# Performance work log

Hardware: AMD Instinct MI355X
Metric: run time of the kernel (lower is better)

The kernel has to match this reference:

```python
import jax, jax.numpy as jnp
import numpy as np

LN_EPS = 1e-12


def _layernorm(x, gamma, beta):
    mu = jnp.mean(x, axis=-1, keepdims=True)
    var = jnp.var(x, axis=-1, keepdims=True)
    return gamma * (x - mu) / jnp.sqrt(var + LN_EPS) + beta


def setup_inputs() -> dict:
    key = jax.random.key(0)
    ks = jax.random.split(key, 8)
    B, N, C, H = 8, 8192, 512, 8
    FFN = 4 * C
    s_attn = 1.0 / np.sqrt(C)
    s_ffn1 = 1.0 / np.sqrt(C)
    s_ffn2 = 1.0 / np.sqrt(FFN)
    return {
        "x": jax.random.normal(ks[0], (B, N, C), jnp.float32),
        "wq": jax.random.normal(ks[1], (C, C), jnp.float32) * s_attn,
        "bq": jnp.zeros((C,), jnp.float32),
        "wk": jax.random.normal(ks[2], (C, C), jnp.float32) * s_attn,
        "bk": jnp.zeros((C,), jnp.float32),
        "wv": jax.random.normal(ks[3], (C, C), jnp.float32) * s_attn,
        "bv": jnp.zeros((C,), jnp.float32),
        "wo": jax.random.normal(ks[4], (C, C), jnp.float32) * s_attn,
        "bo": jnp.zeros((C,), jnp.float32),
        "gamma1": jnp.ones((C,), jnp.float32),
        "beta1": jnp.zeros((C,), jnp.float32),
        "w_fc1": jax.random.normal(ks[5], (C, FFN), jnp.float32) * s_ffn1,
        "b_fc1": jnp.zeros((FFN,), jnp.float32),
        "w_fc2": jax.random.normal(ks[6], (FFN, C), jnp.float32) * s_ffn2,
        "b_fc2": jnp.zeros((C,), jnp.float32),
        "gamma2": jnp.ones((C,), jnp.float32),
        "beta2": jnp.zeros((C,), jnp.float32),
        "window_size": 64,
        "n_head": 8,
    }


def reference(x, wq, bq, wk, bk, wv, bv, wo, bo, gamma1, beta1,
              w_fc1, b_fc1, w_fc2, b_fc2, gamma2, beta2,
              window_size, n_head):
    B, N, C = x.shape
    ws = window_size
    H = n_head
    dh = C // H

    # window partition: [B, N, C] -> [B*N/ws, ws, C]
    xw = x.reshape(B * N // ws, ws, C)
    shortcut = xw

    # windowed multi-head self-attention
    q = (xw @ wq + bq).reshape(-1, ws, H, dh)
    k = (xw @ wk + bk).reshape(-1, ws, H, dh)
    v = (xw @ wv + bv).reshape(-1, ws, H, dh)
    scale = 1.0 / jnp.sqrt(jnp.asarray(dh, xw.dtype))
    attn = jnp.einsum('wqhd,wkhd->whqk', q, k) * scale  # [nw, H, ws, ws]
    attn = jax.nn.softmax(attn, axis=-1)
    out = jnp.einsum('whqk,wkhd->wqhd', attn, v).reshape(-1, ws, C)
    out = out @ wo + bo

    # residual + LN1
    h = _layernorm(out + shortcut, gamma1, beta1)

    # MLP (fc1 -> GELU -> fc2), residual + LN2
    ff = jax.nn.gelu(h @ w_fc1 + b_fc1, approximate=False) @ w_fc2 + b_fc2
    h = _layernorm(ff + h, gamma2, beta2)

    # window reverse: -> [B, N, C]
    return h.reshape(B, N, C)
```

## Files before the change

### kernel.cpp

```cpp
#include <hip/hip_runtime.h>

typedef __attribute__((ext_vector_type(8))) short bf16x8;
typedef __attribute__((ext_vector_type(4))) float f32x4;

__device__ __forceinline__ short f2b(float f) {
  unsigned u = __builtin_bit_cast(unsigned, f);
  unsigned r = (u + 0x7FFFu + ((u >> 16) & 1u)) >> 16;
  return (short)r;
}
__device__ __forceinline__ float b2f(short s) {
  unsigned u = ((unsigned)(unsigned short)s) << 16;
  return __builtin_bit_cast(float, u);
}

__device__ __forceinline__ void gload16(const void* g, void* l) {
  __builtin_amdgcn_global_load_lds(
      (const __attribute__((address_space(1))) void*)g,
      (__attribute__((address_space(3))) void*)l, 16, 0, 0);
}

__device__ __forceinline__ float gelu_f(float v) {
  float u = v * (0.7978845608f + 0.0356774081f * v * v);
  float a = fabsf(u);
  float e = __expf(-2.f * a);
  float t = (1.f - e) * __builtin_amdgcn_rcpf(1.f + e);
  t = (u < 0.f) ? -t : t;
  return 0.5f * v * (1.f + t);
}

__global__ void cvt_bf16_vec(const float* __restrict__ src, short* __restrict__ dst, long n) {
  long i = ((long)blockIdx.x * 256 + threadIdx.x) * 8;
  if (i >= n) return;
  f32x4 a = *(const f32x4*)(src + i);
  f32x4 b = *(const f32x4*)(src + i + 4);
  bf16x8 o;
#pragma unroll
  for (int j = 0; j < 4; j++) o[j] = f2b(a[j]);
#pragma unroll
  for (int j = 0; j < 4; j++) o[j + 4] = f2b(b[j]);
  *(bf16x8*)(dst + i) = o;
}

__global__ void transpose_cvt_t(const float* __restrict__ src, short* __restrict__ dst,
                                int K, int N) {
  __shared__ float tile[32][33];
  const int n0 = blockIdx.x * 32, k0 = blockIdx.y * 32;
  const int j = threadIdx.x & 31, i0 = threadIdx.x >> 5;
#pragma unroll
  for (int r = 0; r < 4; r++) {
    int i = i0 + r * 8;
    tile[i][j] = src[(long)(k0 + i) * N + n0 + j];
  }
  __syncthreads();
#pragma unroll
  for (int r = 0; r < 4; r++) {
    int i = i0 + r * 8;
    dst[(long)(n0 + i) * K + k0 + j] = f2b(tile[j][i]);
  }
}

__global__ void pack_bias3(const float* __restrict__ b0, const float* __restrict__ b1,
                           const float* __restrict__ b2, float* __restrict__ out) {
  int t = blockIdx.x * 256 + threadIdx.x;
  if (t >= 1536) return;
  out[t] = (t < 512) ? b0[t] : ((t < 1024) ? b1[t - 512] : b2[t - 1024]);
}

#define DSR(d, a, OFF) \
  asm volatile("ds_read_b128 %0, %1 offset:" OFF : "=v"(d) : "v"(a))
#define SB __builtin_amdgcn_sched_barrier(0)

template <int EPI>
__global__ __launch_bounds__(512, 1) void gemm256(
    const short* __restrict__ A, const short* __restrict__ Bt,
    const float* __restrict__ bias, const float* __restrict__ resF,
    const short* __restrict__ resB, void* __restrict__ Cout, int K, int ldc, int gxN) {
  extern __shared__ short lds[];
  const int t = threadIdx.x;
  const int lane = t & 63, w = t >> 6;
  const int lr = lane & 15, lg = lane >> 4;
  const int wm = w >> 2, wn = w & 3;

  const int nwg = gridDim.x, orig = blockIdx.x;
  const int q8 = nwg >> 3, r8 = nwg & 7, xcd = orig & 7, idx = orig >> 3;
  const int swz = (xcd < r8 ? xcd * (q8 + 1) : r8 * (q8 + 1) + (xcd - r8) * q8) + idx;
  const long m0 = (long)(swz / gxN) * 256;
  const int n0 = (swz % gxN) * 256;

  f32x4 acc[8][4];
#pragma unroll
  for (int i = 0; i < 8; i++)
#pragma unroll
    for (int j = 0; j < 4; j++) acc[i][j] = f32x4{0.f, 0.f, 0.f, 0.f};

  const int srow = t >> 3;
  const int sch = (t & 7) ^ (srow & 7);
  const short* sA = A + (m0 + srow) * (long)K + sch * 8;
  const short* sB = Bt + ((long)n0 + srow) * K + sch * 8;
  const long r64 = (long)64 * K;

#define STG_A(tt, h)                                                     \
  {                                                                      \
    short* d_ = lds + ((tt) & 1) * 16384 + (h) * 8192 + t * 8;           \
    const short* s_ = sA + (h) * 2 * r64 + (long)(tt) * 64;              \
    gload16(s_, d_);                                                     \
    gload16(s_ + r64, d_ + 4096);                                        \
  }
#define STG_B(tt, h)                                                     \
  {                                                                      \
    short* d_ = lds + 32768 + ((tt) & 1) * 16384 + (h) * 8192 + t * 8;   \
    const short* s_ = sB + (h) * 2 * r64 + (long)(tt) * 64;              \
    gload16(s_, d_);                                                     \
    gload16(s_ + r64, d_ + 4096);                                        \
  }

  const unsigned ldsB = (unsigned)(uintptr_t)lds;
  const unsigned xb0 = (unsigned)((lg ^ (lr & 7)) * 16);
  const unsigned xb1 = (unsigned)(((4 + lg) ^ (lr & 7)) * 16);
  const unsigned aRowB = (unsigned)((wm * 128 + lr) * 128);
  const unsigned bRowB = 65536u + (unsigned)((wn * 64 + lr) * 128);

#define BAR                                  \
  {                                          \
    SB;                                      \
    __builtin_amdgcn_s_barrier();            \
    SB;                                      \
  }
#define LGKM0 asm volatile("s_waitcnt lgkmcnt(0)")

  const int NT = K >> 6;
  STG_A(0, 0) STG_A(0, 1) STG_B(0, 0) STG_B(0, 1) STG_B(1, 0) STG_B(1, 1)
  asm volatile("s_waitcnt vmcnt(4)" ::: "memory");
  BAR

#define MFMA8(AC, A0, A1)                                                      \
  {                                                                            \
    __builtin_amdgcn_s_setprio(1);                                             \
    acc[AC][0] = __builtin_amdgcn_mfma_f32_16x16x32_bf16(A0, b00, acc[AC][0], 0, 0, 0); \
    acc[AC][0] = __builtin_amdgcn_mfma_f32_16x16x32_bf16(A1, b01, acc[AC][0], 0, 0, 0); \
    acc[AC][1] = __builtin_amdgcn_mfma_f32_16x16x32_bf16(A0, b10, acc[AC][1], 0, 0, 0); \
    acc[AC][1] = __builtin_amdgcn_mfma_f32_16x16x32_bf16(A1, b11, acc[AC][1], 0, 0, 0); \
    acc[AC][2] = __builtin_amdgcn_mfma_f32_16x16x32_bf16(A0, b20, acc[AC][2], 0, 0, 0); \
    acc[AC][2] = __builtin_amdgcn_mfma_f32_16x16x32_bf16(A1, b21, acc[AC][2], 0, 0, 0); \
    acc[AC][3] = __builtin_amdgcn_mfma_f32_16x16x32_bf16(A0, b30, acc[AC][3], 0, 0, 0); \
    acc[AC][3] = __builtin_amdgcn_mfma_f32_16x16x32_bf16(A1, b31, acc[AC][3], 0, 0, 0); \
    __builtin_amdgcn_s_setprio(0);                                             \
  }

  for (int tt = 0; tt < NT; ++tt) {
    const unsigned dAb = (unsigned)((tt & 1) * 32768);
    const unsigned aA0 = ldsB + aRowB + xb0 + dAb;
    const unsigned aA1 = ldsB + aRowB + xb1 + dAb;
    const unsigned bA0 = ldsB + bRowB + xb0 + dAb;
    const unsigned bA1 = ldsB + bRowB + xb1 + dAb;
    bf16x8 b00, b01, b10, b11, b20, b21, b30, b31;

    {
      DSR(b00, bA0, "0");    DSR(b01, bA1, "0");
      DSR(b10, bA0, "2048"); DSR(b11, bA1, "2048");
      DSR(b20, bA0, "4096"); DSR(b21, bA1, "4096");
      DSR(b30, bA0, "6144"); DSR(b31, bA1, "6144");
      bf16x8 a00, a01, a10, a11;
      DSR(a00, aA0, "0");    DSR(a01, aA1, "0");
      DSR(a10, aA0, "2048"); DSR(a11, aA1, "2048");
      SB;
      if (tt + 1 < NT) STG_A(tt + 1, 0)
      BAR
      LGKM0; SB;
      MFMA8(0, a00, a01)
      MFMA8(1, a10, a11)
      BAR
    }
    {
      bf16x8 a00, a01, a10, a11;
      DSR(a00, aA0, "4096"); DSR(a01, aA1, "4096");
      DSR(a10, aA0, "6144"); DSR(a11, aA1, "6144");
      SB;
      if (tt + 1 < NT) STG_A(tt + 1, 1)
      BAR
      LGKM0; SB;
      MFMA8(2, a00, a01)
      MFMA8(3, a10, a11)
      BAR
    }
    {
      bf16x8 a00, a01, a10, a11;
      DSR(a00, aA0, "8192");  DSR(a01, aA1, "8192");
      DSR(a10, aA0, "10240"); DSR(a11, aA1, "10240");
      SB;
      if (tt + 2 < NT) STG_B(tt + 2, 0)
      BAR
      LGKM0; SB;
      MFMA8(4, a00, a01)
      MFMA8(5, a10, a11)
      BAR
    }
    {
      bf16x8 a00, a01, a10, a11;
      DSR(a00, aA0, "12288"); DSR(a01, aA1, "12288");
      DSR(a10, aA0, "14336"); DSR(a11, aA1, "14336");
      SB;
      if (tt + 2 < NT) STG_B(tt + 2, 1)
      BAR
      LGKM0; SB;
      MFMA8(6, a00, a01)
      MFMA8(7, a10, a11)
      if (tt + 2 < NT) {
        asm volatile("s_waitcnt vmcnt(4)" ::: "memory");
      } else if (tt + 1 < NT) {
        asm volatile("s_waitcnt vmcnt(0)" ::: "memory");
      }
      BAR
    }
  }
#undef MFMA8
#undef STG_A
#undef STG_B

  float bv[4];
#pragma unroll
  for (int nj = 0; nj < 4; nj++) bv[nj] = bias[n0 + wn * 64 + nj * 16 + lr];

#pragma unroll
  for (int a = 0; a < 8; a++)
#pragma unroll
    for (int i = 0; i < 4; i++) {
      const long row = m0 + wm * 128 + a * 16 + lg * 4 + i;
      const long rb = row * ldc + n0 + wn * 64 + lr;
      if (EPI == 0) {
        short* p = (short*)Cout + rb;
#pragma unroll
        for (int nj = 0; nj < 4; nj++) p[nj * 16] = f2b(acc[a][nj][i] + bv[nj]);
      } else if (EPI == 1) {
        short* p = (short*)Cout + rb;
#pragma unroll
        for (int nj = 0; nj < 4; nj++) p[nj * 16] = f2b(gelu_f(acc[a][nj][i] + bv[nj]));
      } else if (EPI == 2) {
        float* p = (float*)Cout + rb;
        const float* rp = resF + rb;
#pragma unroll
        for (int nj = 0; nj < 4; nj++) p[nj * 16] = acc[a][nj][i] + bv[nj] + rp[nj * 16];
      } else {
        float* p = (float*)Cout + rb;
        const short* rp = resB + rb;
#pragma unroll
        for (int nj = 0; nj < 4; nj++)
          p[nj * 16] = acc[a][nj][i] + bv[nj] + b2f(rp[nj * 16]);
      }
    }
}
#undef DSR
#undef SB
#undef BAR
#undef LGKM0

__global__ __launch_bounds__(256, 2) void attn_win(const short* __restrict__ QKV,
                                                   short* __restrict__ AO) {
  __shared__ short Vs[64 * 72];
  __shared__ short Ps[64 * 72];
  const int t = threadIdx.x, w = t >> 6, lane = t & 63;
  const int lr = lane & 15, lg = lane >> 4;
  const long base = (long)blockIdx.x * 64 * 1536;
  const long obase = (long)blockIdx.x * 64 * 512;

  for (int h = 0; h < 8; h++) {
    const int co = h * 64;
#pragma unroll
    for (int it = 0; it < 2; it++) {
      int c = t + it * 256;
      int j = c >> 3, d0 = (c & 7) * 8;
      *(bf16x8*)(Vs + j * 72 + d0) =
          *(const bf16x8*)(QKV + base + (long)j * 1536 + 1024 + co + d0);
    }
    __syncthreads();

    bf16x8 qf[2], kf[4][2];
#pragma unroll
    for (int kb = 0; kb < 2; kb++)
      qf[kb] = *(const bf16x8*)(QKV + base + (long)(w * 16 + lr) * 1536 + co + kb * 32 + lg * 8);
#pragma unroll
    for (int nj = 0; nj < 4; nj++)
#pragma unroll
      for (int kb = 0; kb < 2; kb++)
        kf[nj][kb] = *(const bf16x8*)(QKV + base + (long)(nj * 16 + lr) * 1536 + 512 + co +
                                      kb * 32 + lg * 8);

    f32x4 s[4];
#pragma unroll
    for (int nj = 0; nj < 4; nj++) {
      s[nj] = f32x4{0.f, 0.f, 0.f, 0.f};
      s[nj] = __builtin_amdgcn_mfma_f32_16x16x32_bf16(qf[0], kf[nj][0], s[nj], 0, 0, 0);
      s[nj] = __builtin_amdgcn_mfma_f32_16x16x32_bf16(qf[1], kf[nj][1], s[nj], 0, 0, 0);
      s[nj] = s[nj] * 0.125f;
    }

#pragma unroll
    for (int i = 0; i < 4; i++) {
      float mx = fmaxf(fmaxf(s[0][i], s[1][i]), fmaxf(s[2][i], s[3][i]));
#pragma unroll
      for (int off = 1; off < 16; off <<= 1) mx = fmaxf(mx, __shfl_xor(mx, off, 64));
      float sum = 0.f;
#pragma unroll
      for (int nj = 0; nj < 4; nj++) {
        float p = __expf(s[nj][i] - mx);
        s[nj][i] = p;
        sum += p;
      }
#pragma unroll
      for (int off = 1; off < 16; off <<= 1) sum += __shfl_xor(sum, off, 64);
      float inv = 1.f / sum;
#pragma unroll
      for (int nj = 0; nj < 4; nj++) s[nj][i] *= inv;
    }

#pragma unroll
    for (int nj = 0; nj < 4; nj++)
#pragma unroll
      for (int i = 0; i < 4; i++)
        Ps[(w * 16 + lg * 4 + i) * 72 + nj * 16 + lr] = f2b(s[nj][i]);

    bf16x8 pa[2];
#pragma unroll
    for (int kb = 0; kb < 2; kb++)
      pa[kb] = *(const bf16x8*)(Ps + (w * 16 + lr) * 72 + kb * 32 + lg * 8);

    f32x4 o[4];
#pragma unroll
    for (int nb = 0; nb < 4; nb++) o[nb] = f32x4{0.f, 0.f, 0.f, 0.f};
#pragma unroll
    for (int kb = 0; kb < 2; kb++)
#pragma unroll
      for (int nb = 0; nb < 4; nb++) {
        bf16x8 vb;
#pragma unroll
        for (int jj = 0; jj < 8; jj++)
          vb[jj] = Vs[(kb * 32 + lg * 8 + jj) * 72 + nb * 16 + lr];
        o[nb] = __builtin_amdgcn_mfma_f32_16x16x32_bf16(pa[kb], vb, o[nb], 0, 0, 0);
      }

#pragma unroll
    for (int nb = 0; nb < 4; nb++)
#pragma unroll
      for (int i = 0; i < 4; i++)
        AO[obase + (long)(w * 16 + lg * 4 + i) * 512 + co + nb * 16 + lr] = f2b(o[nb][i]);
    __syncthreads();
  }
}

template <int OUTB>
__global__ __launch_bounds__(256, 4) void ln_rows(const float* __restrict__ Y,
                                                  const float* __restrict__ gamma,
                                                  const float* __restrict__ beta,
                                                  short* __restrict__ Hb,
                                                  float* __restrict__ Of) {
  const int w = threadIdx.x >> 6, lane = threadIdx.x & 63;
  const long row = (long)blockIdx.x * 4 + w;
  const float* y = Y + row * 512 + lane * 8;
  f32x4 a = *(const f32x4*)(y);
  f32x4 b = *(const f32x4*)(y + 4);
  float s = a[0] + a[1] + a[2] + a[3] + b[0] + b[1] + b[2] + b[3];
  float s2 = a[0] * a[0] + a[1] * a[1] + a[2] * a[2] + a[3] * a[3] + b[0] * b[0] +
             b[1] * b[1] + b[2] * b[2] + b[3] * b[3];
#pragma unroll
  for (int off = 1; off < 64; off <<= 1) {
    s += __shfl_xor(s, off, 64);
    s2 += __shfl_xor(s2, off, 64);
  }
  float mu = s * (1.f / 512.f);
  float var = s2 * (1.f / 512.f) - mu * mu;
  float rstd = rsqrtf(fmaxf(var, 0.f) + 1e-12f);
  const int c0 = lane * 8;
  f32x4 ga = *(const f32x4*)(gamma + c0), gb = *(const f32x4*)(gamma + c0 + 4);
  f32x4 ba = *(const f32x4*)(beta + c0), bb = *(const f32x4*)(beta + c0 + 4);
  if (OUTB) {
    bf16x8 o;
#pragma unroll
    for (int j = 0; j < 4; j++) o[j] = f2b(ga[j] * ((a[j] - mu) * rstd) + ba[j]);
#pragma unroll
    for (int j = 0; j < 4; j++) o[j + 4] = f2b(gb[j] * ((b[j] - mu) * rstd) + bb[j]);
    *(bf16x8*)(Hb + row * 512 + c0) = o;
  } else {
    f32x4 o0, o1;
#pragma unroll
    for (int j = 0; j < 4; j++) o0[j] = ga[j] * ((a[j] - mu) * rstd) + ba[j];
#pragma unroll
    for (int j = 0; j < 4; j++) o1[j] = gb[j] * ((b[j] - mu) * rstd) + bb[j];
    *(f32x4*)(Of + row * 512 + c0) = o0;
    *(f32x4*)(Of + row * 512 + c0 + 4) = o1;
  }
}

extern "C" void kernel_launch(void* const* d_in, const int* in_sizes, int n_in,
                              void* d_out, int out_size, void* d_ws, size_t ws_size,
                              hipStream_t stream) {
  (void)in_sizes; (void)n_in; (void)out_size;
  const float* x = (const float*)d_in[0];
  const float* wq = (const float*)d_in[1];
  const float* bq = (const float*)d_in[2];
  const float* wk = (const float*)d_in[3];
  const float* bk = (const float*)d_in[4];
  const float* wv = (const float*)d_in[5];
  const float* bv = (const float*)d_in[6];
  const float* wo = (const float*)d_in[7];
  const float* bo = (const float*)d_in[8];
  const float* g1 = (const float*)d_in[9];
  const float* be1 = (const float*)d_in[10];
  const float* wfc1 = (const float*)d_in[11];
  const float* bfc1 = (const float*)d_in[12];
  const float* wfc2 = (const float*)d_in[13];
  const float* bfc2 = (const float*)d_in[14];
  const float* g2 = (const float*)d_in[15];
  const float* be2 = (const float*)d_in[16];

  const long T = 65536;
  char* ws = (char*)d_ws;

  short* WQKVT = (short*)(ws);
  short* WOT = WQKVT + 1536 * 512;
  short* WFC1T = WOT + 512 * 512;
  short* WFC2T = WFC1T + 2048 * 512;
  float* BQKV = (float*)(WFC2T + 512 * 2048);
  size_t woff = ((size_t)((char*)(BQKV + 1536) - ws) + 255) & ~(size_t)255;

  size_t avail = (ws_size > woff) ? (ws_size - woff) : 0;
  long Tc = T;
  while (Tc > 256 && (size_t)Tc * 7168 > avail) Tc >>= 1;
  const long nch = T / Tc;

  char* R0 = ws + woff;
  char* R1 = R0 + (size_t)Tc * 4096;
  char* R2 = R1 + (size_t)Tc * 2048;

  short* QKV = (short*)R0;
  float* Y1 = (float*)R0;
  short* FF1 = (short*)R0;
  short* XB = (short*)R1;
  short* AO = (short*)R1;
  float* Y2 = (float*)R1;
  short* H = (short*)R2;

  transpose_cvt_t<<<dim3(16, 16), 256, 0, stream>>>(wq, WQKVT, 512, 512);
  transpose_cvt_t<<<dim3(16, 16), 256, 0, stream>>>(wk, WQKVT + 512 * 512, 512, 512);
  transpose_cvt_t<<<dim3(16, 16), 256, 0, stream>>>(wv, WQKVT + 1024 * 512, 512, 512);
  transpose_cvt_t<<<dim3(16, 16), 256, 0, stream>>>(wo, WOT, 512, 512);
  transpose_cvt_t<<<dim3(64, 16), 256, 0, stream>>>(wfc1, WFC1T, 512, 2048);
  transpose_cvt_t<<<dim3(16, 64), 256, 0, stream>>>(wfc2, WFC2T, 2048, 512);
  pack_bias3<<<6, 256, 0, stream>>>(bq, bk, bv, BQKV);

  const size_t LDSB = 131072;
  for (long c = 0; c < nch; c++) {
    const long t0 = c * Tc;
    const int mb = (int)(Tc / 256);
    cvt_bf16_vec<<<(int)(Tc / 4), 256, 0, stream>>>(x + t0 * 512, XB, Tc * 512);
    gemm256<0><<<mb * 6, 512, LDSB, stream>>>(XB, WQKVT, BQKV, nullptr, nullptr,
                                              (void*)QKV, 512, 1536, 6);
    attn_win<<<(int)(Tc / 64), 256, 0, stream>>>(QKV, AO);
    gemm256<2><<<mb * 2, 512, LDSB, stream>>>(AO, WOT, bo, x + t0 * 512, nullptr,
                                              (void*)Y1, 512, 512, 2);
    ln_rows<1><<<(int)(Tc / 4), 256, 0, stream>>>(Y1, g1, be1, H, nullptr);
    gemm256<1><<<mb * 8, 512, LDSB, stream>>>(H, WFC1T, bfc1, nullptr, nullptr,
                                              (void*)FF1, 512, 2048, 8);
    gemm256<3><<<mb * 2, 512, LDSB, stream>>>(FF1, WFC2T, bfc2, nullptr, H, (void*)Y2,
                                              2048, 512, 2);
    ln_rows<0><<<(int)(Tc / 4), 256, 0, stream>>>(Y2, g2, be2, nullptr,
                                                  (float*)d_out + t0 * 512);
  }
}
```

Measured before the change: 772.0 us.

## Add 128x128 triple-buffered GEMM for FC1 and store pre-LN1 sum in bf16

Adds a new 256-thread GEMM with 128x128 tiles and a three-stage LDS ring fed by direct global-to-LDS loads, and uses it for the FC1 projection in place of the 256x256 kernel. The smaller tiles give more workgroups, aiming at better occupancy and load balance. The attention-output GEMM now writes the residual sum as bf16 instead of fp32, and LN1 reads bf16, which halves that intermediate's traffic. The cost is lower precision for the LN1 input.

```diff
diff --git a/kernel.cpp b/kernel.cpp
--- a/kernel.cpp
+++ b/kernel.cpp
@@ -64,6 +64,123 @@
   int t = blockIdx.x * 256 + threadIdx.x;
   if (t >= 1536) return;
   out[t] = (t < 512) ? b0[t] : ((t < 1024) ? b1[t - 512] : b2[t - 1024]);
+}
+
+template <int EPI>
+__global__ __launch_bounds__(256, 3) void gemm_bt(
+    const short* __restrict__ A, const short* __restrict__ Bt,
+    const float* __restrict__ bias, const float* __restrict__ resF,
+    const short* __restrict__ resB, void* __restrict__ Cout, int K, int ldc, int gxN) {
+  __shared__ short lds[3 * 8192];
+  const int t = threadIdx.x;
+  const int w = t >> 6, lane = t & 63;
+  const int lr = lane & 15, lg = lane >> 4;
+
+  const int nwg = gridDim.x;
+  const int orig = blockIdx.x;
+  const int q = nwg >> 3, r = nwg & 7, xcd = orig & 7, idx = orig >> 3;
+  const int swz = (xcd < r ? xcd * (q + 1) : r * (q + 1) + (xcd - r) * q) + idx;
+  const long m0 = (long)(swz / gxN) * 128;
+  const int n0 = (swz % gxN) * 128;
+
+  const int wm = (w >> 1) * 64, wn = (w & 1) * 64;
+
+  f32x4 acc[4][4];
+#pragma unroll
+  for (int i = 0; i < 4; i++)
+#pragma unroll
+    for (int j = 0; j < 4; j++) acc[i][j] = f32x4{0.f, 0.f, 0.f, 0.f};
+
+  const int srow = t >> 2;
+  const int schunk = (t & 3) ^ ((t >> 3) & 3);
+  const short* Ag = A + (m0 + srow) * (long)K + schunk * 8;
+  const short* Bg = Bt + ((long)n0 + srow) * K + schunk * 8;
+  const long half = (long)64 * K;
+
+#define STAGE(b, kt)                                   \
+  {                                                    \
+    short* d = lds + (b) * 8192 + t * 8;               \
+    gload16(Ag + (long)(kt) * 32, d);                  \
+    gload16(Ag + half + (long)(kt) * 32, d + 2048);    \
+    gload16(Bg + (long)(kt) * 32, d + 4096);           \
+    gload16(Bg + half + (long)(kt) * 32, d + 6144);    \
+  }
+
+  const int xsw = (lg ^ ((lr >> 1) & 3)) * 8;
+  const int aoff = (wm + lr) * 32 + xsw;
+  const int boff = 4096 + (wn + lr) * 32 + xsw;
+
+#define TILE_WAIT(WN)                                        \
+  asm volatile("s_waitcnt vmcnt(" #WN ")" ::: "memory");     \
+  __builtin_amdgcn_sched_barrier(0);                         \
+  __builtin_amdgcn_s_barrier();                              \
+  __builtin_amdgcn_sched_barrier(0);
+
+#define BODY(CB)                                                               \
+  {                                                                            \
+    const short* Lb = lds + (CB) * 8192;                                       \
+    bf16x8 a[4], b[4];                                                         \
+    _Pragma("unroll") for (int mi = 0; mi < 4; mi++)                           \
+        a[mi] = *(const bf16x8*)(Lb + aoff + mi * 512);                        \
+    _Pragma("unroll") for (int nj = 0; nj < 4; nj++)                           \
+        b[nj] = *(const bf16x8*)(Lb + boff + nj * 512);                        \
+    __builtin_amdgcn_s_setprio(1);                                             \
+    _Pragma("unroll") for (int mi = 0; mi < 4; mi++)                           \
+        _Pragma("unroll") for (int nj = 0; nj < 4; nj++) acc[mi][nj] =         \
+            __builtin_amdgcn_mfma_f32_16x16x32_bf16(a[mi], b[nj], acc[mi][nj], \
+                                                    0, 0, 0);                  \
+    __builtin_amdgcn_s_setprio(0);                                             \
+  }
+
+  const int NKT = K >> 5;
+  STAGE(0, 0)
+  STAGE(1, 1)
+
+  int cb = 0, sb = 2;
+  for (int kt = 0; kt < NKT - 1; ++kt) {
+    TILE_WAIT(4)
+    if (kt + 2 < NKT) STAGE(sb, kt + 2)
+    BODY(cb)
+    cb = (cb == 2) ? 0 : cb + 1;
+    sb = (sb == 2) ? 0 : sb + 1;
+  }
+  TILE_WAIT(0)
+  BODY(cb)
+#undef STAGE
+#undef TILE_WAIT
+#undef BODY
+
+  float bv[4];
+#pragma unroll
+  for (int nj = 0; nj < 4; nj++) bv[nj] = bias[n0 + wn + nj * 16 + lr];
+
+#pragma unroll
+  for (int mi = 0; mi < 4; mi++)
+#pragma unroll
+    for (int i = 0; i < 4; i++) {
+      const long row = m0 + wm + mi * 16 + lg * 4 + i;
+      const long rb = row * ldc + n0 + wn + lr;
+      if (EPI == 0) {
+        short* p = (short*)Cout + rb;
+#pragma unroll
+        for (int nj = 0; nj < 4; nj++) p[nj * 16] = f2b(acc[mi][nj][i] + bv[nj]);
+      } else if (EPI == 1) {
+        short* p = (short*)Cout + rb;
+#pragma unroll
+        for (int nj = 0; nj < 4; nj++) p[nj * 16] = f2b(gelu_f(acc[mi][nj][i] + bv[nj]));
+      } else if (EPI == 2) {
+        short* p = (short*)Cout + rb;
+        const float* rp = resF + rb;
+#pragma unroll
+        for (int nj = 0; nj < 4; nj++) p[nj * 16] = f2b(acc[mi][nj][i] + bv[nj] + rp[nj * 16]);
+      } else {
+        float* p = (float*)Cout + rb;
+        const short* rp = resB + rb;
+#pragma unroll
+        for (int nj = 0; nj < 4; nj++)
+          p[nj * 16] = acc[mi][nj][i] + bv[nj] + b2f(rp[nj * 16]);
+      }
+    }
 }
 
 #define DSR(d, a, OFF) \
@@ -236,10 +353,11 @@
 #pragma unroll
         for (int nj = 0; nj < 4; nj++) p[nj * 16] = f2b(gelu_f(acc[a][nj][i] + bv[nj]));
       } else if (EPI == 2) {
-        float* p = (float*)Cout + rb;
+        short* p = (short*)Cout + rb;
         const float* rp = resF + rb;
 #pragma unroll
-        for (int nj = 0; nj < 4; nj++) p[nj * 16] = acc[a][nj][i] + bv[nj] + rp[nj * 16];
+        for (int nj = 0; nj < 4; nj++)
+          p[nj * 16] = f2b(acc[a][nj][i] + bv[nj] + rp[nj * 16]);
       } else {
         float* p = (float*)Cout + rb;
         const short* rp = resB + rb;
@@ -347,20 +465,29 @@
   }
 }
 
-template <int OUTB>
-__global__ __launch_bounds__(256, 4) void ln_rows(const float* __restrict__ Y,
+template <int INB, int OUTB>
+__global__ __launch_bounds__(256, 4) void ln_rows(const float* __restrict__ Yf,
+                                                  const short* __restrict__ Yb,
                                                   const float* __restrict__ gamma,
                                                   const float* __restrict__ beta,
                                                   short* __restrict__ Hb,
                                                   float* __restrict__ Of) {
   const int w = threadIdx.x >> 6, lane = threadIdx.x & 63;
   const long row = (long)blockIdx.x * 4 + w;
-  const float* y = Y + row * 512 + lane * 8;
-  f32x4 a = *(const f32x4*)(y);
-  f32x4 b = *(const f32x4*)(y + 4);
-  float s = a[0] + a[1] + a[2] + a[3] + b[0] + b[1] + b[2] + b[3];
-  float s2 = a[0] * a[0] + a[1] * a[1] + a[2] * a[2] + a[3] * a[3] + b[0] * b[0] +
-             b[1] * b[1] + b[2] * b[2] + b[3] * b[3];
+  float v[8];
+  if (INB) {
+    bf16x8 x = *(const bf16x8*)(Yb + row * 512 + lane * 8);
+#pragma unroll
+    for (int j = 0; j < 8; j++) v[j] = b2f(x[j]);
+  } else {
+    f32x4 a = *(const f32x4*)(Yf + row * 512 + lane * 8);
+    f32x4 b = *(const f32x4*)(Yf + row * 512 + lane * 8 + 4);
+#pragma unroll
+    for (int j = 0; j < 4; j++) { v[j] = a[j]; v[j + 4] = b[j]; }
+  }
+  float s = 0.f, s2 = 0.f;
+#pragma unroll
+  for (int j = 0; j < 8; j++) { s += v[j]; s2 += v[j] * v[j]; }
 #pragma unroll
   for (int off = 1; off < 64; off <<= 1) {
     s += __shfl_xor(s, off, 64);
@@ -375,16 +502,16 @@
   if (OUTB) {
     bf16x8 o;
 #pragma unroll
-    for (int j = 0; j < 4; j++) o[j] = f2b(ga[j] * ((a[j] - mu) * rstd) + ba[j]);
-#pragma unroll
-    for (int j = 0; j < 4; j++) o[j + 4] = f2b(gb[j] * ((b[j] - mu) * rstd) + bb[j]);
+    for (int j = 0; j < 4; j++) o[j] = f2b(ga[j] * ((v[j] - mu) * rstd) + ba[j]);
+#pragma unroll
+    for (int j = 0; j < 4; j++) o[j + 4] = f2b(gb[j] * ((v[j + 4] - mu) * rstd) + bb[j]);
     *(bf16x8*)(Hb + row * 512 + c0) = o;
   } else {
     f32x4 o0, o1;
 #pragma unroll
-    for (int j = 0; j < 4; j++) o0[j] = ga[j] * ((a[j] - mu) * rstd) + ba[j];
-#pragma unroll
-    for (int j = 0; j < 4; j++) o1[j] = gb[j] * ((b[j] - mu) * rstd) + bb[j];
+    for (int j = 0; j < 4; j++) o0[j] = ga[j] * ((v[j] - mu) * rstd) + ba[j];
+#pragma unroll
+    for (int j = 0; j < 4; j++) o1[j] = gb[j] * ((v[j + 4] - mu) * rstd) + bb[j];
     *(f32x4*)(Of + row * 512 + c0) = o0;
     *(f32x4*)(Of + row * 512 + c0 + 4) = o1;
   }
@@ -432,7 +559,7 @@
   char* R2 = R1 + (size_t)Tc * 2048;
 
   short* QKV = (short*)R0;
-  float* Y1 = (float*)R0;
+  short* Y1b = (short*)R0;
   short* FF1 = (short*)R0;
   short* XB = (short*)R1;
   short* AO = (short*)R1;
@@ -451,18 +578,19 @@
   for (long c = 0; c < nch; c++) {
     const long t0 = c * Tc;
     const int mb = (int)(Tc / 256);
+    const int mb2 = (int)(Tc / 128);
     cvt_bf16_vec<<<(int)(Tc / 4), 256, 0, stream>>>(x + t0 * 512, XB, Tc * 512);
     gemm256<0><<<mb * 6, 512, LDSB, stream>>>(XB, WQKVT, BQKV, nullptr, nullptr,
                                               (void*)QKV, 512, 1536, 6);
     attn_win<<<(int)(Tc / 64), 256, 0, stream>>>(QKV, AO);
     gemm256<2><<<mb * 2, 512, LDSB, stream>>>(AO, WOT, bo, x + t0 * 512, nullptr,
-                                              (void*)Y1, 512, 512, 2);
-    ln_rows<1><<<(int)(Tc / 4), 256, 0, stream>>>(Y1, g1, be1, H, nullptr);
-    gemm256<1><<<mb * 8, 512, LDSB, stream>>>(H, WFC1T, bfc1, nullptr, nullptr,
-                                              (void*)FF1, 512, 2048, 8);
+                                              (void*)Y1b, 512, 512, 2);
+    ln_rows<1, 1><<<(int)(Tc / 4), 256, 0, stream>>>(nullptr, Y1b, g1, be1, H, nullptr);
+    gemm_bt<1><<<mb2 * 16, 256, 0, stream>>>(H, WFC1T, bfc1, nullptr, nullptr,
+                                             (void*)FF1, 512, 2048, 16);
     gemm256<3><<<mb * 2, 512, LDSB, stream>>>(FF1, WFC2T, bfc2, nullptr, H, (void*)Y2,
                                               2048, 512, 2);
-    ln_rows<0><<<(int)(Tc / 4), 256, 0, stream>>>(Y2, g2, be2, nullptr,
-                                                  (float*)d_out + t0 * 512);
-  }
-}
+    ln_rows<0, 0><<<(int)(Tc / 4), 256, 0, stream>>>(Y2, nullptr, g2, be2, nullptr,
+                                                     (float*)d_out + t0 * 512);
+  }
+}
```

New measurement: 761.6 us. About the same (-1.3%).
